# Kernel tuning notes

Measured on AMD Instinct MI355X. Metric: run time of the kernel, lower is better.

Reference implementation:

```python
import jax, jax.numpy as jnp
import numpy as np

B, P, S = 128, 10, 8
L, BF = 81, 75
OF, MF2 = 40, 20
C = 64
H = 3 * C  # hidden_size = 192
NCHAR = 8
EPS = 1e-5


def setup_inputs() -> dict:
    key = jax.random.key(0)
    ks = jax.random.split(key, 24)
    n = lambda i, shp: jax.random.normal(ks[i], shp, jnp.float32)
    w = lambda i, shp: jax.random.normal(ks[i], shp, jnp.float32) * 0.02
    return {
        "board": n(0, (B, P, S, L, BF)),
        "order": n(1, (B, P, S, OF)),
        "message": n(2, (B, P, S, MF2)),
        "other_ind": jax.random.uniform(ks[3], (B, P, 7), jnp.float32),
        "me_ind": jax.random.uniform(ks[4], (B, P, 7), jnp.float32),
        "h0": n(5, (P, B, H)),
        "c0": n(6, (P, B, H)),
        "Wb1": w(7, (1024, L * BF)), "bb1": jnp.zeros((1024,), jnp.float32),
        "Wb2": w(8, (256, 1024)), "bb2": jnp.zeros((256,), jnp.float32),
        "Wb3": w(9, (C, 256)), "bb3": jnp.zeros((C,), jnp.float32),
        "Wo1": w(10, (128, OF)), "bo1": jnp.zeros((128,), jnp.float32),
        "Wo2": w(11, (32, 128)), "bo2": jnp.zeros((32,), jnp.float32),
        "Wo3": w(12, (C, 32)), "bo3": jnp.zeros((C,), jnp.float32),
        "Wm1": w(13, (64, MF2)), "bm1": jnp.zeros((64,), jnp.float32),
        "Wm2": w(14, (32, 64)), "bm2": jnp.zeros((32,), jnp.float32),
        "Wm3": w(15, (C, 32)), "bm3": jnp.zeros((C,), jnp.float32),
        "g1": jnp.ones((C,), jnp.float32), "be1": jnp.zeros((C,), jnp.float32),
        "g2": jnp.ones((C,), jnp.float32), "be2": jnp.zeros((C,), jnp.float32),
        "g3": jnp.ones((C,), jnp.float32), "be3": jnp.zeros((C,), jnp.float32),
        "Wih": w(16, (4 * H, H)), "Whh": w(17, (4 * H, H)),
        "bih": jnp.zeros((4 * H,), jnp.float32), "bhh": jnp.zeros((4 * H,), jnp.float32),
        "Wf1": w(18, (256, S * H)), "bf1": jnp.zeros((256,), jnp.float32),
        "Wf2": w(19, (NCHAR, 256 + 14)), "bf2": jnp.zeros((NCHAR,), jnp.float32),
    }


def _mlp3(x, W1, b1, W2, b2, W3, b3):
    x = jax.nn.relu(x @ W1.T + b1)
    x = jax.nn.relu(x @ W2.T + b2)
    return x @ W3.T + b3


def _bn_relu(x, g, b):
    # x: [b, C, S]; BatchNorm1d in training mode -> biased batch stats over (N, L)
    m = x.mean(axis=(0, 2), keepdims=True)
    v = jnp.mean((x - m) ** 2, axis=(0, 2), keepdims=True)
    return jax.nn.relu(g[None, :, None] * (x - m) * jax.lax.rsqrt(v + EPS) + b[None, :, None])


def _forward(board, order, message, other_ind, me_ind, h0, c0,
             Wb1, bb1, Wb2, bb2, Wb3, bb3, Wo1, bo1, Wo2, bo2, Wo3, bo3,
             Wm1, bm1, Wm2, bm2, Wm3, bm3, g1, be1, g2, be2, g3, be3,
             Wih, Whh, bih, bhh, Wf1, bf1, Wf2, bf2):
    num_step = board.shape[2]

    def per_past(board_p, order_p, msg_p, oi_p, mi_p, h, c):
        bb = board_p.shape[0]
        bf = _mlp3(board_p.reshape(bb * num_step, -1), Wb1, bb1, Wb2, bb2, Wb3, bb3)
        bf = _bn_relu(jnp.swapaxes(bf.reshape(bb, num_step, -1), 1, 2), g1, be1)
        of = _mlp3(order_p.reshape(bb * num_step, -1), Wo1, bo1, Wo2, bo2, Wo3, bo3)
        of = _bn_relu(jnp.swapaxes(of.reshape(bb, num_step, -1), 1, 2), g2, be2)
        mf = _mlp3(msg_p.reshape(bb * num_step, -1), Wm1, bm1, Wm2, bm2, Wm3, bm3)
        mf = _bn_relu(jnp.swapaxes(mf.reshape(bb, num_step, -1), 1, 2), g3, be3)
        x_feat = jnp.concatenate([bf, of, mf], axis=-1)              # [b, C, 3S]
        x_feat = jnp.transpose(jnp.swapaxes(x_feat, 1, 2), (2, 0, 1))  # [C, b, 3S]
        x_feat = x_feat.reshape(num_step, bb, -1)                    # [S, b, H] (same C-order reindex as torch)

        def step(carry, xt):
            h_, c_ = carry
            gates = xt @ Wih.T + bih + h_ @ Whh.T + bhh
            i, f, g_, o = jnp.split(gates, 4, axis=-1)
            c_ = jax.nn.sigmoid(f) * c_ + jax.nn.sigmoid(i) * jnp.tanh(g_)
            h_ = jax.nn.sigmoid(o) * jnp.tanh(c_)
            return (h_, c_), h_

        _, outs = jax.lax.scan(step, (h, c), x_feat)  # [S, b, H]
        x = jnp.swapaxes(outs, 0, 1).reshape(bb, -1)  # [b, S*H]
        x = jax.nn.relu(x @ Wf1.T + bf1)
        x = jnp.concatenate([x, oi_p, mi_p], axis=-1)  # [b, 256+14]
        return x @ Wf2.T + bf2

    per = jax.vmap(per_past)(
        jnp.swapaxes(board, 0, 1), jnp.swapaxes(order, 0, 1), jnp.swapaxes(message, 0, 1),
        jnp.swapaxes(other_ind, 0, 1), jnp.swapaxes(me_ind, 0, 1), h0, c0)  # [P, b, NCHAR]
    return per.sum(axis=0)


def reference(board, order, message, other_ind, me_ind, h0, c0,
              Wb1, bb1, Wb2, bb2, Wb3, bb3, Wo1, bo1, Wo2, bo2, Wo3, bo3,
              Wm1, bm1, Wm2, bm2, Wm3, bm3, g1, be1, g2, be2, g3, be3,
              Wih, Whh, bih, bhh, Wf1, bf1, Wf2, bf2):
    return _forward(board, order, message, other_ind, me_ind, h0, c0,
                    Wb1, bb1, Wb2, bb2, Wb3, bb3, Wo1, bo1, Wo2, bo2, Wo3, bo3,
                    Wm1, bm1, Wm2, bm2, Wm3, bm3, g1, be1, g2, be2, g3, be3,
                    Wih, Whh, bih, bhh, Wf1, bf1, Wf2, bf2)
```

## Files before the change

kernel.cpp:

```cpp
#include <hip/hip_runtime.h>
#include <stdint.h>

typedef unsigned short u16;
typedef __bf16 v8bf __attribute__((ext_vector_type(8)));
typedef float  v4f  __attribute__((ext_vector_type(4)));

__device__ __forceinline__ u16 f2bf(float f) {
    union { float f; unsigned u; } x; x.f = f;
    unsigned r = (x.u + 0x7FFFu + ((x.u >> 16) & 1u)) >> 16;
    return (u16)r;
}
__device__ __forceinline__ float sigf(float x) { return 1.f / (1.f + __expf(-x)); }
__device__ __forceinline__ void gload(const u16* src, u16* ldst) {
    __builtin_amdgcn_global_load_lds((const __attribute__((address_space(1))) void*)src,
                                     (__attribute__((address_space(3))) void*)ldst, 16, 0, 0);
}

#define OFF_ABF    0UL
#define OFF_XINBF  0UL
#define OFF_XG     3932160UL
#define OFF_FC1    44728320UL
#define OFF_WB1    125829120UL
#define OFF_C1     138412032UL
#define OFF_WB2    159383552UL
#define OFF_WB3    165150720UL
#define OFF_BFE    165216256UL
#define OFF_OFE    167837696UL
#define OFF_MFE    170459136UL
#define OFF_WIH    173095936UL
#define OFF_WHH    173390848UL
#define OFF_WF1    173685760UL
#define OFF_BSUM   174472192UL

__global__ void __launch_bounds__(256) conv_board(const float* __restrict__ src, u16* __restrict__ dst)
{
    int bid = blockIdx.x;
    int row = bid / 6, chunk = bid - row * 6;
    int k0 = chunk * 1024 + threadIdx.x * 4;
    const float* s = src + (long)row * 6075 + k0;
    u16* d = dst + (long)row * 6144 + k0;
    if (k0 + 4 <= 6075) {
        float f0 = s[0], f1 = s[1], f2 = s[2], f3 = s[3];
        uint2 v;
        v.x = (unsigned)f2bf(f0) | ((unsigned)f2bf(f1) << 16);
        v.y = (unsigned)f2bf(f2) | ((unsigned)f2bf(f3) << 16);
        *(uint2*)d = v;
    } else {
#pragma unroll
        for (int z = 0; z < 4; ++z) {
            int k = k0 + z;
            d[z] = f2bf(k < 6075 ? s[z] : 0.f);
        }
    }
}

__global__ void __launch_bounds__(256) conv_weights(
    const float* __restrict__ Wb1, const float* __restrict__ Wb2, const float* __restrict__ Wb3,
    const float* __restrict__ Wih, const float* __restrict__ Whh, const float* __restrict__ Wf1,
    const float* __restrict__ bih, const float* __restrict__ bhh,
    u16* __restrict__ dWb1, u16* __restrict__ dWb2, u16* __restrict__ dWb3,
    u16* __restrict__ dWih, u16* __restrict__ dWhh, u16* __restrict__ dWf1,
    float* __restrict__ bsum)
{
    const long C0 = 6291456, C1 = 6553600, C2 = 6586368, C3 = 6733824,
               C4 = 6881280, C5 = 7274496, C6 = 7275264;
    for (long i = (long)blockIdx.x * 256 + threadIdx.x; i < C6; i += (long)gridDim.x * 256) {
        if (i < C0) {
            int r = (int)(i / 6144), k = (int)(i % 6144);
            dWb1[i] = f2bf(k < 6075 ? Wb1[(long)r * 6075 + k] : 0.f);
        } else if (i < C1) {
            long j = i - C0;
            dWb2[j] = f2bf(Wb2[j]);
        } else if (i < C2) {
            long j = i - C1;
            dWb3[j] = f2bf(j < 16384 ? Wb3[j] : 0.f);
        } else if (i < C3) {
            long j = i - C2;
            dWih[j] = f2bf(Wih[j]);
        } else if (i < C4) {
            long j = i - C3;
            dWhh[j] = f2bf(Whh[j]);
        } else if (i < C5) {
            long j = i - C4;
            dWf1[j] = f2bf(Wf1[j]);
        } else {
            long j = i - C5;
            bsum[j] = bih[j] + bhh[j];
        }
    }
}

#define G160_LDS 106496
__global__ void __launch_bounds__(512, 1)
gemm160(const u16* __restrict__ A, const u16* __restrict__ B,
        const float* __restrict__ bias, u16* __restrict__ C, int K)
{
    extern __shared__ __align__(16) u16 smem[];
    const int tid = threadIdx.x, wv = tid >> 6, lane = tid & 63;
    const int bid = blockIdx.x;
    const int col = bid >> 6, rowt = bid & 63;
    const long m0 = (long)rowt * 160;
    const long n0 = (long)col * 256;

    const int sr8 = lane >> 3;
    const int sslot = (lane & 7) ^ sr8;
    const u16* Ag = A + (m0 + wv * 8 + sr8) * (long)K + sslot * 8;
    const u16* Bg = B + (n0 + wv * 8 + sr8) * (long)K + sslot * 8;
    const int wr = wv >> 2, wc = wv & 3;
    const int wm = wr * 80, wn = wc * 64;
    const int fr = lane & 15, hi = lane >> 4, fx = fr & 7;

    const int nk = K >> 6;
    v4f acc[5][4] = {};

    auto STAGE = [&](int buf, int t) {
        const long k0 = (long)t * 64;
        const int ab = buf * 26624;
#pragma unroll
        for (int r = 0; r < 2; ++r)
            gload(Ag + (long)r * 64 * K + k0, smem + ab + r * 4096 + wv * 512);
        if (wv < 4)
            gload(Ag + (long)128 * K + k0, smem + ab + 8192 + wv * 512);
#pragma unroll
        for (int r = 0; r < 4; ++r)
            gload(Bg + (long)r * 64 * K + k0, smem + ab + 10240 + r * 4096 + wv * 512);
    };
    auto LDA_ = [&](int buf, int ks, int i) -> v8bf {
        return *(const v8bf*)(smem + buf * 26624 + (wm + i * 16 + fr) * 64 + ((ks * 4 + hi) ^ fx) * 8);
    };
    auto LDB_ = [&](int buf, int ks, int j) -> v8bf {
        return *(const v8bf*)(smem + buf * 26624 + 10240 + (wn + j * 16 + fr) * 64 + ((ks * 4 + hi) ^ fx) * 8);
    };

    STAGE(0, 0);
    STAGE(1, 1);
    for (int t = 0; t < nk; ++t) {
        const int buf = t & 1;
        if (t + 1 < nk) { asm volatile("s_waitcnt vmcnt(6)" ::: "memory"); }
        else            { asm volatile("s_waitcnt vmcnt(0)" ::: "memory"); }
        asm volatile("s_barrier" ::: "memory");
        __builtin_amdgcn_s_setprio(1);
        v8bf a0[5], a1[5], b0[4], b1[4];
#pragma unroll
        for (int j = 0; j < 4; ++j) b0[j] = LDB_(buf, 0, j);
#pragma unroll
        for (int i = 0; i < 5; ++i) a0[i] = LDA_(buf, 0, i);
        __builtin_amdgcn_sched_barrier(0);
#pragma unroll
        for (int j = 0; j < 4; ++j) b1[j] = LDB_(buf, 1, j);
#pragma unroll
        for (int i = 0; i < 5; ++i) a1[i] = LDA_(buf, 1, i);
#pragma unroll
        for (int i = 0; i < 5; ++i)
#pragma unroll
            for (int j = 0; j < 4; ++j)
                acc[i][j] = __builtin_amdgcn_mfma_f32_16x16x32_bf16(a0[i], b0[j], acc[i][j], 0, 0, 0);
        __builtin_amdgcn_sched_barrier(0);
        __builtin_amdgcn_s_setprio(0);
        asm volatile("s_waitcnt lgkmcnt(0)" ::: "memory");
        __builtin_amdgcn_sched_barrier(0);
        asm volatile("s_barrier" ::: "memory");
        if (t + 2 < nk) STAGE(buf, t + 2);
        __builtin_amdgcn_s_setprio(1);
#pragma unroll
        for (int i = 0; i < 5; ++i)
#pragma unroll
            for (int j = 0; j < 4; ++j)
                acc[i][j] = __builtin_amdgcn_mfma_f32_16x16x32_bf16(a1[i], b1[j], acc[i][j], 0, 0, 0);
        __builtin_amdgcn_s_setprio(0);
    }

#pragma unroll
    for (int i = 0; i < 5; ++i) {
        const long mr = m0 + wm + i * 16 + hi * 4;
#pragma unroll
        for (int j = 0; j < 4; ++j) {
            const long n = n0 + wn + j * 16 + fr;
            float bv = bias[n];
#pragma unroll
            for (int r = 0; r < 4; ++r) {
                float v = fmaxf(acc[i][j][r] + bv, 0.f);
                C[(mr + r) * 1024L + n] = f2bf(v);
            }
        }
    }
}

#define L23_LDS 98304
__global__ void __launch_bounds__(512, 1)
gemm_l23(const u16* __restrict__ A, const u16* __restrict__ B, const float* __restrict__ b2,
         const u16* __restrict__ W3, const float* __restrict__ b3, float* __restrict__ Out)
{
    extern __shared__ __align__(16) u16 smem[];
    const int tid = threadIdx.x, wv = tid >> 6, lane = tid & 63;
    const long m0 = (long)blockIdx.x * 128;
    const int sr8 = lane >> 3;
    const int sslot = (lane & 7) ^ sr8;
    const u16* Ag = A + (m0 + wv * 8 + sr8) * 1024L + sslot * 8;
    const u16* Bg = B + (wv * 8 + sr8) * 1024L + sslot * 8;
    const int wr = wv >> 2, wc = wv & 3;
    const int wm = wr * 64, wn = wc * 64;
    const int fr = lane & 15, hi = lane >> 4, fx = fr & 7;

    v4f acc[4][4] = {};

    auto STAGE = [&](int buf, int t) {
        const long k0 = (long)t * 64;
        const int ab = buf * 24576;
#pragma unroll
        for (int r = 0; r < 2; ++r)
            gload(Ag + (long)r * 64 * 1024 + k0, smem + ab + r * 4096 + wv * 512);
#pragma unroll
        for (int r = 0; r < 4; ++r)
            gload(Bg + (long)r * 64 * 1024 + k0, smem + ab + 8192 + r * 4096 + wv * 512);
    };
    auto COMPUTE = [&](int buf) {
#pragma unroll
        for (int ks = 0; ks < 2; ++ks) {
            const int sw = ((ks * 4 + hi) ^ fx) * 8;
            v8bf a[4], b[4];
#pragma unroll
            for (int i = 0; i < 4; ++i)
                a[i] = *(const v8bf*)(smem + buf * 24576 + (wm + i * 16 + fr) * 64 + sw);
#pragma unroll
            for (int j = 0; j < 4; ++j)
                b[j] = *(const v8bf*)(smem + buf * 24576 + 8192 + (wn + j * 16 + fr) * 64 + sw);
#pragma unroll
            for (int i = 0; i < 4; ++i)
#pragma unroll
                for (int j = 0; j < 4; ++j)
                    acc[i][j] = __builtin_amdgcn_mfma_f32_16x16x32_bf16(a[i], b[j], acc[i][j], 0, 0, 0);
        }
    };

    STAGE(0, 0);
    __syncthreads();
    int t = 1;
    while (true) {
        if (t < 16) STAGE(1, t);
        COMPUTE(0);
        if (t >= 16) break;
        __syncthreads();
        ++t;
        if (t < 16) STAGE(0, t);
        COMPUTE(1);
        if (t >= 16) break;
        __syncthreads();
        ++t;
    }
    __syncthreads();
    u16* C2s = smem;
#pragma unroll
    for (int i = 0; i < 4; ++i) {
        const int rrow = wm + i * 16 + hi * 4;
#pragma unroll
        for (int j = 0; j < 4; ++j) {
            const int ccol = wn + j * 16 + fr;
            float bv = b2[ccol];
#pragma unroll
            for (int r = 0; r < 4; ++r)
                C2s[(rrow + r) * 264 + ccol] = f2bf(fmaxf(acc[i][j][r] + bv, 0.f));
        }
    }
    __syncthreads();
    v4f a3[4] = {};
#pragma unroll
    for (int kk = 0; kk < 8; ++kk) {
        v8bf af = *(const v8bf*)(&C2s[(wv * 16 + fr) * 264 + kk * 32 + hi * 8]);
#pragma unroll
        for (int j = 0; j < 4; ++j) {
            v8bf bfr = *(const v8bf*)(W3 + (j * 16 + fr) * 256 + kk * 32 + hi * 8);
            a3[j] = __builtin_amdgcn_mfma_f32_16x16x32_bf16(af, bfr, a3[j], 0, 0, 0);
        }
    }
#pragma unroll
    for (int j = 0; j < 4; ++j) {
        int n = j * 16 + fr;
        float bv = b3[n];
#pragma unroll
        for (int q = 0; q < 4; ++q)
            Out[(m0 + wv * 16 + hi * 4 + q) * 64 + n] = a3[j][q] + bv;
    }
}

template<int OBF, int RELU, int BIAS>
__global__ void __launch_bounds__(256)
gemm_bt(const u16* __restrict__ A, const u16* __restrict__ B,
        const float* __restrict__ bias, void* __restrict__ Cv,
        int M, int N, int K, int ldc)
{
    __shared__ __align__(16) u16 As[2][128 * 64];
    __shared__ __align__(16) u16 Bs[2][128 * 64];
    const int tid = threadIdx.x;
    const int wv = tid >> 6, lane = tid & 63;
    const long m0 = (long)blockIdx.y * 128;
    const long n0 = (long)blockIdx.x * 128;
    const int srow  = wv * 8 + (lane >> 3);
    const int sslot = (lane & 7) ^ (lane >> 3);
    const u16* Ag = A + (m0 + srow) * (long)K + sslot * 8;
    const u16* Bg = B + (n0 + srow) * (long)K + sslot * 8;
    const int wm = (wv >> 1) * 64, wn = (wv & 1) * 64;
    const int fr = lane & 15, hi = lane >> 4;
    const int fx = fr & 7;

    v4f acc[4][4] = {};
    const int nk = K >> 6;

    auto STAGE = [&](int buf, int k0) {
#pragma unroll
        for (int r = 0; r < 4; ++r)
            gload(Ag + (long)r * 32 * K + k0, &As[buf][r * 2048 + wv * 512]);
#pragma unroll
        for (int r = 0; r < 4; ++r)
            gload(Bg + (long)r * 32 * K + k0, &Bs[buf][r * 2048 + wv * 512]);
    };
    auto COMPUTE = [&](int buf) {
#pragma unroll
        for (int ks = 0; ks < 2; ++ks) {
            v8bf a[4], b[4];
            const int sw = (((ks * 4 + hi) ^ fx)) * 8;
#pragma unroll
            for (int i = 0; i < 4; ++i)
                a[i] = *(const v8bf*)(&As[buf][(wm + i * 16 + fr) * 64 + sw]);
#pragma unroll
            for (int j = 0; j < 4; ++j)
                b[j] = *(const v8bf*)(&Bs[buf][(wn + j * 16 + fr) * 64 + sw]);
#pragma unroll
            for (int i = 0; i < 4; ++i)
#pragma unroll
                for (int j = 0; j < 4; ++j)
                    acc[i][j] = __builtin_amdgcn_mfma_f32_16x16x32_bf16(a[i], b[j], acc[i][j], 0, 0, 0);
        }
    };

    STAGE(0, 0);
    __syncthreads();
    int t = 1;
    while (true) {
        if (t < nk) STAGE(1, t * 64);
        COMPUTE(0);
        if (t >= nk) break;
        __syncthreads();
        ++t;
        if (t < nk) STAGE(0, t * 64);
        COMPUTE(1);
        if (t >= nk) break;
        __syncthreads();
        ++t;
    }

#pragma unroll
    for (int i = 0; i < 4; ++i) {
        const long mr = m0 + wm + i * 16 + hi * 4;
#pragma unroll
        for (int j = 0; j < 4; ++j) {
            const long n = n0 + wn + j * 16 + fr;
            if (n < N) {
                float bv = BIAS ? bias[n] : 0.f;
#pragma unroll
                for (int r = 0; r < 4; ++r) {
                    float v = acc[i][j][r] + bv;
                    if (RELU) v = fmaxf(v, 0.f);
                    if (OBF) ((u16*)Cv)[(mr + r) * (long)ldc + n] = f2bf(v);
                    else     ((float*)Cv)[(mr + r) * (long)ldc + n] = v;
                }
            }
        }
    }
}

template<int D0, int D1>
__global__ void __launch_bounds__(256)
mlp3_small(const float* __restrict__ X,
           const float* __restrict__ W1, const float* __restrict__ B1,
           const float* __restrict__ W2, const float* __restrict__ B2,
           const float* __restrict__ W3, const float* __restrict__ B3,
           float* __restrict__ Out)
{
    __shared__ float w1s[D0 * D1];
    __shared__ float w2s[D1 * 32];
    __shared__ float w3s[32 * 64];
    __shared__ float b1s[D1], b2s[32], b3s[64];
    __shared__ float xs[32 * D0];
    __shared__ float h1[32 * D1];
    __shared__ float h2[32 * 32];

    const int tid = threadIdx.x;
    const long row0 = (long)blockIdx.x * 32;

    for (int i = tid; i < D0 * D1; i += 256) { int k = i / D1, n = i % D1; w1s[i] = W1[n * D0 + k]; }
    for (int i = tid; i < D1 * 32; i += 256) { int k = i / 32,  n = i % 32; w2s[i] = W2[n * D1 + k]; }
    for (int i = tid; i < 32 * 64; i += 256) { int k = i / 64,  n = i % 64; w3s[i] = W3[n * 32 + k]; }
    if (tid < D1) b1s[tid] = B1[tid];
    if (tid < 32) b2s[tid] = B2[tid];
    if (tid < 64) b3s[tid] = B3[tid];
    for (int i = tid; i < 32 * D0; i += 256) xs[i] = X[(row0 + i / D0) * D0 + i % D0];
    __syncthreads();

    const int wv = tid >> 6, lane = tid & 63;
    const int r0 = wv * 8;
    {
        constexpr int NL = D1 / 64;
        float acc[NL][8];
#pragma unroll
        for (int a = 0; a < NL; ++a)
#pragma unroll
            for (int r = 0; r < 8; ++r) acc[a][r] = 0.f;
        for (int k = 0; k < D0; ++k) {
            float w[NL];
#pragma unroll
            for (int a = 0; a < NL; ++a) w[a] = w1s[k * D1 + lane + a * 64];
#pragma unroll
            for (int r = 0; r < 8; ++r) {
                float x = xs[(r0 + r) * D0 + k];
#pragma unroll
                for (int a = 0; a < NL; ++a) acc[a][r] += w[a] * x;
            }
        }
#pragma unroll
        for (int a = 0; a < NL; ++a)
#pragma unroll
            for (int r = 0; r < 8; ++r)
                h1[(r0 + r) * D1 + lane + a * 64] = fmaxf(acc[a][r] + b1s[lane + a * 64], 0.f);
    }
    __syncthreads();
    {
        int n = lane & 31;
        int rb = r0 + (lane >> 5) * 4;
        float acc[4] = {0, 0, 0, 0};
        for (int k = 0; k < D1; ++k) {
            float w = w2s[k * 32 + n];
#pragma unroll
            for (int r = 0; r < 4; ++r) acc[r] += w * h1[(rb + r) * D1 + k];
        }
#pragma unroll
        for (int r = 0; r < 4; ++r) h2[(rb + r) * 32 + n] = fmaxf(acc[r] + b2s[n], 0.f);
    }
    __syncthreads();
    {
        float acc[8] = {};
        for (int k = 0; k < 32; ++k) {
            float w = w3s[k * 64 + lane];
#pragma unroll
            for (int r = 0; r < 8; ++r) acc[r] += w * h2[(r0 + r) * 32 + k];
        }
#pragma unroll
        for (int r = 0; r < 8; ++r) Out[(row0 + r0 + r) * 64 + lane] = acc[r] + b3s[lane];
    }
}

#define BX_LDS 100032
__global__ void __launch_bounds__(256, 1)
build_xin2(const float* __restrict__ bfe, const float* __restrict__ ofe, const float* __restrict__ mfe,
           const float* __restrict__ g1, const float* __restrict__ be1,
           const float* __restrict__ g2, const float* __restrict__ be2,
           const float* __restrict__ g3, const float* __restrict__ be3,
           u16* __restrict__ xin)
{
    extern __shared__ __align__(16) float ls[];
    float* coefA = ls + 24576;
    float* coefB = coefA + 24;
    float* psum  = coefB + 24;
    float* psum2 = psum + 192;
    const int p = blockIdx.x >> 3, s = blockIdx.x & 7;
    const int tid = threadIdx.x;
    const float* Fs[3] = {bfe, ofe, mfe};
    for (int g = tid; g < 3072; g += 256) {
        int br = g >> 10, rr = g & 1023, bb = rr >> 3, tt = rr & 7;
        const float* srcp = Fs[br] + ((long)(bb * 80 + p * 8 + tt)) * 64 + s * 8;
        float4 v0 = *(const float4*)srcp;
        float4 v1 = *(const float4*)(srcp + 4);
        *(float4*)(ls + (long)g * 8) = v0;
        *(float4*)(ls + (long)g * 8 + 4) = v1;
    }
    __syncthreads();
    if (tid < 192) {
        int pair = tid >> 3, part = tid & 7;
        int br = pair >> 3, cl = pair & 7;
        float s1 = 0.f, s2 = 0.f;
        for (int b2 = 0; b2 < 16; ++b2) {
            int bb = part * 16 + b2;
            const float* base = ls + ((br * 128 + bb) * 8) * 8 + cl;
#pragma unroll
            for (int tt = 0; tt < 8; ++tt) { float v = base[tt * 8]; s1 += v; s2 += v * v; }
        }
        psum[tid] = s1; psum2[tid] = s2;
    }
    __syncthreads();
    if (tid < 24) {
        float s1 = 0.f, s2 = 0.f;
#pragma unroll
        for (int q = 0; q < 8; ++q) { s1 += psum[tid * 8 + q]; s2 += psum2[tid * 8 + q]; }
        int br = tid >> 3, cl = tid & 7, c = s * 8 + cl;
        const float* G  = br == 0 ? g1  : (br == 1 ? g2  : g3);
        const float* BE = br == 0 ? be1 : (br == 1 ? be2 : be3);
        float m  = s1 * (1.f / 1024.f);
        float var = s2 * (1.f / 1024.f) - m * m;
        float Aa = G[c] * rsqrtf(var + 1e-5f);
        coefA[tid] = Aa;
        coefB[tid] = BE[c] - Aa * m;
    }
    __syncthreads();
    const int u = tid >> 1, h0 = (tid & 1) * 96;
    const long obase = ((long)(p * 8 + s) * 128 + u) * 192 + h0;
    const int cl = u >> 4;
    const int ub = (u & 15) * 8;
    union { u16 u[8]; uint4 v; } pk;
    for (int hq = 0; hq < 12; ++hq) {
#pragma unroll
        for (int z = 0; z < 8; ++z) {
            int h = h0 + hq * 8 + z;
            int bb = ub + h / 24, t = h % 24, br = t >> 3, tt = t & 7;
            float v = ls[((br * 128 + bb) * 8 + tt) * 8 + cl];
            float r = fmaxf(v * coefA[br * 8 + cl] + coefB[br * 8 + cl], 0.f);
            pk.u[z] = f2bf(r);
        }
        *(uint4*)(xin + obase + hq * 8) = pk.v;
    }
}

#define LSTM_LDS (98304 + 6400 + 49152)
__global__ void __launch_bounds__(512, 1)
lstm_persist(const float* __restrict__ Xg, const u16* __restrict__ Whh,
             const float* __restrict__ h0, const float* __restrict__ c0,
             const u16* __restrict__ Wf1, const float* __restrict__ bf1,
             float* __restrict__ fc1o)
{
    extern __shared__ __align__(16) u16 smem[];
    u16*   WT    = smem;
    u16*   hS    = smem + 2 * 128 * 192;
    float* gates = (float*)(smem + 2 * 128 * 192 + 16 * 200);

    const int tid = threadIdx.x, wv = tid >> 6, lane = tid & 63;
    const int R0 = blockIdx.x * 16;
    const int fr = lane & 15, hi = lane >> 4;

    for (int i = tid; i < 16 * 200; i += 512) {
        int r = i / 200, cx = i % 200;
        hS[i] = (cx < 192) ? f2bf(h0[(R0 + r) * 192 + cx]) : (u16)0;
    }
    float creg[6];
#pragma unroll
    for (int j = 0; j < 6; ++j) {
        int e = j * 512 + tid;
        creg[j] = c0[(R0 + e / 192) * 192 + e % 192];
    }

    auto WSTAGE = [&](int buf, int it) {
#pragma unroll
        for (int q = 0; q < 6; ++q) {
            int g = q * 512 + tid;
            int row = g / 24, sl = g % 24;
            const u16* src = Whh + (long)(it * 128 + row) * 192 + (sl ^ (row & 7)) * 8;
            gload(src, WT + buf * 24576 + q * 4096 + wv * 512);
        }
    };
    auto NITER = [&](int buf, int nt, const v8bf* a) {
        int row = wv * 16 + fr;
        v4f acc = {};
#pragma unroll
        for (int ks = 0; ks < 6; ++ks) {
            v8bf b = *(const v8bf*)(&WT[buf * 24576 + row * 192 + ((ks * 4 + hi) ^ (fr & 7)) * 8]);
            acc = __builtin_amdgcn_mfma_f32_16x16x32_bf16(a[ks], b, acc, 0, 0, 0);
        }
        int n = nt * 128 + row;
#pragma unroll
        for (int q = 0; q < 4; ++q)
            gates[(hi * 4 + q) * 768 + n] = acc[q];
    };

    v4f f1acc[2] = {};
    const int nb0 = wv * 32;
    auto WF1ACC = [&](int ss, const v8bf* a) {
#pragma unroll
        for (int jf = 0; jf < 2; ++jf) {
            v4f tacc = f1acc[jf];
#pragma unroll
            for (int ks = 0; ks < 6; ++ks) {
                v8bf bfr = *(const v8bf*)(Wf1 + (long)(nb0 + jf * 16 + fr) * 1536 + ss * 192 + ks * 32 + hi * 8);
                tacc = __builtin_amdgcn_mfma_f32_16x16x32_bf16(a[ks], bfr, tacc, 0, 0, 0);
            }
            f1acc[jf] = tacc;
        }
    };

    WSTAGE(0, 0);
    for (int s = 0; s < 8; ++s) {
        __syncthreads();
        v8bf a[6];
#pragma unroll
        for (int ks = 0; ks < 6; ++ks)
            a[ks] = *(const v8bf*)(&hS[fr * 200 + ks * 32 + hi * 8]);
        if (s > 0) WF1ACC(s - 1, a);
        int it = 0;
#pragma unroll 1
        for (int pr = 0; pr < 3; ++pr) {
            WSTAGE(1, it + 1);
            NITER(0, it, a);
            __syncthreads();
            if (it + 2 < 6) WSTAGE(0, it + 2);
            else if (s < 7) WSTAGE(0, 0);
            NITER(1, it + 1, a);
            __syncthreads();
            it += 2;
        }
#pragma unroll
        for (int j = 0; j < 6; ++j) {
            int e = j * 512 + tid;
            int r = e / 192, hd = e % 192;
            int grow = R0 + r;
            int p = grow >> 7, u = grow & 127;
            long xrow = (long)((p * 8 + s) * 128 + u) * 768;
            float gi = Xg[xrow + hd]       + gates[r * 768 + hd];
            float gf = Xg[xrow + 192 + hd] + gates[r * 768 + 192 + hd];
            float gg = Xg[xrow + 384 + hd] + gates[r * 768 + 384 + hd];
            float go = Xg[xrow + 576 + hd] + gates[r * 768 + 576 + hd];
            float c = sigf(gf) * creg[j] + sigf(gi) * tanhf(gg);
            float h = sigf(go) * tanhf(c);
            creg[j] = c;
            hS[r * 200 + hd] = f2bf(h);
        }
    }
    __syncthreads();
    {
        v8bf a[6];
#pragma unroll
        for (int ks = 0; ks < 6; ++ks)
            a[ks] = *(const v8bf*)(&hS[fr * 200 + ks * 32 + hi * 8]);
        WF1ACC(7, a);
    }
#pragma unroll
    for (int jf = 0; jf < 2; ++jf)
#pragma unroll
        for (int q = 0; q < 4; ++q) {
            int row = hi * 4 + q;
            int n = nb0 + jf * 16 + fr;
            fc1o[(long)(R0 + row) * 256 + n] = fmaxf(f1acc[jf][q] + bf1[n], 0.f);
        }
}

__global__ void __launch_bounds__(256) final_fc2(
    const float* __restrict__ fc1, const float* __restrict__ oi, const float* __restrict__ mi,
    const float* __restrict__ Wf2, const float* __restrict__ bf2, float* __restrict__ out)
{
    const int wv = threadIdx.x >> 6, lane = threadIdx.x & 63;
    const int w = blockIdx.x * 4 + wv;
    const int u = w >> 3, n = w & 7;
    const float* wrow = Wf2 + n * 270;
    float wreg[4];
#pragma unroll
    for (int q = 0; q < 4; ++q) wreg[q] = wrow[lane + 64 * q];
    float wtail = (lane < 14) ? wrow[256 + lane] : 0.f;
    float acc = 0.f;
    for (int p = 0; p < 10; ++p) {
        const float* x = fc1 + (long)(p * 128 + u) * 256;
#pragma unroll
        for (int q = 0; q < 4; ++q) acc += x[lane + 64 * q] * wreg[q];
        float t = 0.f;
        if (lane < 7)       t = oi[(u * 10 + p) * 7 + lane];
        else if (lane < 14) t = mi[(u * 10 + p) * 7 + lane - 7];
        acc += t * wtail;
    }
#pragma unroll
    for (int off = 32; off; off >>= 1) acc += __shfl_xor(acc, off);
    if (lane == 0) out[u * 8 + n] = acc + bf2[n];
}

extern "C" void kernel_launch(void* const* d_in, const int* in_sizes, int n_in,
                              void* d_out, int out_size, void* d_ws, size_t ws_size,
                              hipStream_t stream)
{
    (void)in_sizes; (void)n_in; (void)out_size; (void)ws_size;
    const float* board = (const float*)d_in[0];
    const float* order = (const float*)d_in[1];
    const float* mess  = (const float*)d_in[2];
    const float* oi    = (const float*)d_in[3];
    const float* mi    = (const float*)d_in[4];
    const float* h0    = (const float*)d_in[5];
    const float* c0    = (const float*)d_in[6];
    const float* Wb1 = (const float*)d_in[7];  const float* bb1 = (const float*)d_in[8];
    const float* Wb2 = (const float*)d_in[9];  const float* bb2 = (const float*)d_in[10];
    const float* Wb3 = (const float*)d_in[11]; const float* bb3 = (const float*)d_in[12];
    const float* Wo1 = (const float*)d_in[13]; const float* bo1 = (const float*)d_in[14];
    const float* Wo2 = (const float*)d_in[15]; const float* bo2 = (const float*)d_in[16];
    const float* Wo3 = (const float*)d_in[17]; const float* bo3 = (const float*)d_in[18];
    const float* Wm1 = (const float*)d_in[19]; const float* bm1 = (const float*)d_in[20];
    const float* Wm2 = (const float*)d_in[21]; const float* bm2 = (const float*)d_in[22];
    const float* Wm3 = (const float*)d_in[23]; const float* bm3 = (const float*)d_in[24];
    const float* g1  = (const float*)d_in[25]; const float* be1 = (const float*)d_in[26];
    const float* g2  = (const float*)d_in[27]; const float* be2 = (const float*)d_in[28];
    const float* g3  = (const float*)d_in[29]; const float* be3 = (const float*)d_in[30];
    const float* Wih = (const float*)d_in[31]; const float* Whh = (const float*)d_in[32];
    const float* bih = (const float*)d_in[33]; const float* bhh = (const float*)d_in[34];
    const float* Wf1 = (const float*)d_in[35]; const float* bf1 = (const float*)d_in[36];
    const float* Wf2 = (const float*)d_in[37]; const float* bf2 = (const float*)d_in[38];

    uint8_t* ws = (uint8_t*)d_ws;
    u16*   A_bf    = (u16*)(ws + OFF_ABF);
    u16*   xin_bf  = (u16*)(ws + OFF_XINBF);
    float* Xg      = (float*)(ws + OFF_XG);
    float* fc1o    = (float*)(ws + OFF_FC1);
    u16*   Wb1_bf  = (u16*)(ws + OFF_WB1);
    u16*   C1_bf   = (u16*)(ws + OFF_C1);
    u16*   Wb2_bf  = (u16*)(ws + OFF_WB2);
    u16*   Wb3_bf  = (u16*)(ws + OFF_WB3);
    float* bfe     = (float*)(ws + OFF_BFE);
    float* ofe     = (float*)(ws + OFF_OFE);
    float* mfe     = (float*)(ws + OFF_MFE);
    u16*   Wih_bf  = (u16*)(ws + OFF_WIH);
    u16*   Whh_bf  = (u16*)(ws + OFF_WHH);
    u16*   Wf1_bf  = (u16*)(ws + OFF_WF1);
    float* bsum    = (float*)(ws + OFF_BSUM);

    conv_board<<<61440, 256, 0, stream>>>(board, A_bf);
    conv_weights<<<2048, 256, 0, stream>>>(Wb1, Wb2, Wb3, Wih, Whh, Wf1, bih, bhh,
                                           Wb1_bf, Wb2_bf, Wb3_bf, Wih_bf, Whh_bf, Wf1_bf, bsum);

    hipFuncSetAttribute(reinterpret_cast<const void*>(gemm160),
                        hipFuncAttributeMaxDynamicSharedMemorySize, G160_LDS);
    gemm160<<<256, 512, G160_LDS, stream>>>(A_bf, Wb1_bf, bb1, C1_bf, 6144);
    hipFuncSetAttribute(reinterpret_cast<const void*>(gemm_l23),
                        hipFuncAttributeMaxDynamicSharedMemorySize, L23_LDS);
    gemm_l23<<<80, 512, L23_LDS, stream>>>(C1_bf, Wb2_bf, bb2, Wb3_bf, bb3, bfe);

    mlp3_small<40, 128><<<320, 256, 0, stream>>>(order, Wo1, bo1, Wo2, bo2, Wo3, bo3, ofe);
    mlp3_small<20, 64><<<320, 256, 0, stream>>>(mess,  Wm1, bm1, Wm2, bm2, Wm3, bm3, mfe);

    hipFuncSetAttribute(reinterpret_cast<const void*>(build_xin2),
                        hipFuncAttributeMaxDynamicSharedMemorySize, BX_LDS);
    build_xin2<<<80, 256, BX_LDS, stream>>>(bfe, ofe, mfe, g1, be1, g2, be2, g3, be3, xin_bf);

    gemm_bt<0, 0, 1><<<dim3(6, 80), 256, 0, stream>>>(xin_bf, Wih_bf, bsum, Xg, 10240, 768, 192, 768);

    hipFuncSetAttribute(reinterpret_cast<const void*>(lstm_persist),
                        hipFuncAttributeMaxDynamicSharedMemorySize, LSTM_LDS);
    lstm_persist<<<80, 512, LSTM_LDS, stream>>>(Xg, Whh_bf, h0, c0, Wf1_bf, bf1, fc1o);

    final_fc2<<<256, 256, 0, stream>>>(fc1o, oi, mi, Wf2, bf2, (float*)d_out);
}
```

Before: 410.2 us.

## Keep LSTM recurrent weights in registers and retile board GEMM for two blocks per CU

The LSTM kernel now loads its per-wave slice of Whh into registers once (36 bf16 fragments per lane) and drops the per-timestep double-buffered LDS staging, along with most barriers inside the recurrence. The first board GEMM is retiled from 512-thread blocks with 160x256 tiles to 256-thread blocks with 160x128 tiles, using less LDS and launch bounds that allow two blocks per CU. Both changes aim to cut memory traffic and synchronisation stalls. The risks are register pressure and spilling in the LSTM kernel, and doubled B-matrix reloads or changed vmcnt accounting in the GEMM.

Measured after the change: 412.1 us. No clear change (+0.5%).

```diff
diff --git a/kernel.cpp b/kernel.cpp
--- a/kernel.cpp
+++ b/kernel.cpp
@@ -90,23 +90,23 @@
     }
 }
 
-#define G160_LDS 106496
-__global__ void __launch_bounds__(512, 1)
+#define G160_LDS 73728
+__global__ void __launch_bounds__(256, 2)
 gemm160(const u16* __restrict__ A, const u16* __restrict__ B,
         const float* __restrict__ bias, u16* __restrict__ C, int K)
 {
     extern __shared__ __align__(16) u16 smem[];
     const int tid = threadIdx.x, wv = tid >> 6, lane = tid & 63;
     const int bid = blockIdx.x;
-    const int col = bid >> 6, rowt = bid & 63;
+    const int col = bid & 7, rowt = bid >> 3;
     const long m0 = (long)rowt * 160;
-    const long n0 = (long)col * 256;
+    const long n0 = (long)col * 128;
 
     const int sr8 = lane >> 3;
     const int sslot = (lane & 7) ^ sr8;
     const u16* Ag = A + (m0 + wv * 8 + sr8) * (long)K + sslot * 8;
     const u16* Bg = B + (n0 + wv * 8 + sr8) * (long)K + sslot * 8;
-    const int wr = wv >> 2, wc = wv & 3;
+    const int wr = wv >> 1, wc = wv & 1;
     const int wm = wr * 80, wn = wc * 64;
     const int fr = lane & 15, hi = lane >> 4, fx = fr & 7;
 
@@ -115,28 +115,26 @@
 
     auto STAGE = [&](int buf, int t) {
         const long k0 = (long)t * 64;
-        const int ab = buf * 26624;
-#pragma unroll
-        for (int r = 0; r < 2; ++r)
-            gload(Ag + (long)r * 64 * K + k0, smem + ab + r * 4096 + wv * 512);
-        if (wv < 4)
-            gload(Ag + (long)128 * K + k0, smem + ab + 8192 + wv * 512);
+        const int ab = buf * 18432;
+#pragma unroll
+        for (int r = 0; r < 5; ++r)
+            gload(Ag + (long)r * 32 * K + k0, smem + ab + r * 2048 + wv * 512);
 #pragma unroll
         for (int r = 0; r < 4; ++r)
-            gload(Bg + (long)r * 64 * K + k0, smem + ab + 10240 + r * 4096 + wv * 512);
+            gload(Bg + (long)r * 32 * K + k0, smem + ab + 10240 + r * 2048 + wv * 512);
     };
     auto LDA_ = [&](int buf, int ks, int i) -> v8bf {
-        return *(const v8bf*)(smem + buf * 26624 + (wm + i * 16 + fr) * 64 + ((ks * 4 + hi) ^ fx) * 8);
+        return *(const v8bf*)(smem + buf * 18432 + (wm + i * 16 + fr) * 64 + ((ks * 4 + hi) ^ fx) * 8);
     };
     auto LDB_ = [&](int buf, int ks, int j) -> v8bf {
-        return *(const v8bf*)(smem + buf * 26624 + 10240 + (wn + j * 16 + fr) * 64 + ((ks * 4 + hi) ^ fx) * 8);
+        return *(const v8bf*)(smem + buf * 18432 + 10240 + (wn + j * 16 + fr) * 64 + ((ks * 4 + hi) ^ fx) * 8);
     };
 
     STAGE(0, 0);
     STAGE(1, 1);
     for (int t = 0; t < nk; ++t) {
         const int buf = t & 1;
-        if (t + 1 < nk) { asm volatile("s_waitcnt vmcnt(6)" ::: "memory"); }
+        if (t + 1 < nk) { asm volatile("s_waitcnt vmcnt(9)" ::: "memory"); }
         else            { asm volatile("s_waitcnt vmcnt(0)" ::: "memory"); }
         asm volatile("s_barrier" ::: "memory");
         __builtin_amdgcn_s_setprio(1);
@@ -519,7 +517,7 @@
     }
 }
 
-#define LSTM_LDS (98304 + 6400 + 49152)
+#define LSTM_LDS (6400 + 49152)
 __global__ void __launch_bounds__(512, 1)
 lstm_persist(const float* __restrict__ Xg, const u16* __restrict__ Whh,
              const float* __restrict__ h0, const float* __restrict__ c0,
@@ -527,14 +525,20 @@
              float* __restrict__ fc1o)
 {
     extern __shared__ __align__(16) u16 smem[];
-    u16*   WT    = smem;
-    u16*   hS    = smem + 2 * 128 * 192;
-    float* gates = (float*)(smem + 2 * 128 * 192 + 16 * 200);
+    u16*   hS    = smem;
+    float* gates = (float*)(smem + 16 * 200);
 
     const int tid = threadIdx.x, wv = tid >> 6, lane = tid & 63;
     const int R0 = blockIdx.x * 16;
     const int fr = lane & 15, hi = lane >> 4;
 
+    v8bf Wreg[6][6];
+#pragma unroll
+    for (int nt = 0; nt < 6; ++nt)
+#pragma unroll
+        for (int ks = 0; ks < 6; ++ks)
+            Wreg[nt][ks] = *(const v8bf*)(Whh + (long)(nt * 128 + wv * 16 + fr) * 192 + ks * 32 + hi * 8);
+
     for (int i = tid; i < 16 * 200; i += 512) {
         int r = i / 200, cx = i % 200;
         hS[i] = (cx < 192) ? f2bf(h0[(R0 + r) * 192 + cx]) : (u16)0;
@@ -545,29 +549,6 @@
         int e = j * 512 + tid;
         creg[j] = c0[(R0 + e / 192) * 192 + e % 192];
     }
-
-    auto WSTAGE = [&](int buf, int it) {
-#pragma unroll
-        for (int q = 0; q < 6; ++q) {
-            int g = q * 512 + tid;
-            int row = g / 24, sl = g % 24;
-            const u16* src = Whh + (long)(it * 128 + row) * 192 + (sl ^ (row & 7)) * 8;
-            gload(src, WT + buf * 24576 + q * 4096 + wv * 512);
-        }
-    };
-    auto NITER = [&](int buf, int nt, const v8bf* a) {
-        int row = wv * 16 + fr;
-        v4f acc = {};
-#pragma unroll
-        for (int ks = 0; ks < 6; ++ks) {
-            v8bf b = *(const v8bf*)(&WT[buf * 24576 + row * 192 + ((ks * 4 + hi) ^ (fr & 7)) * 8]);
-            acc = __builtin_amdgcn_mfma_f32_16x16x32_bf16(a[ks], b, acc, 0, 0, 0);
-        }
-        int n = nt * 128 + row;
-#pragma unroll
-        for (int q = 0; q < 4; ++q)
-            gates[(hi * 4 + q) * 768 + n] = acc[q];
-    };
 
     v4f f1acc[2] = {};
     const int nb0 = wv * 32;
@@ -584,7 +565,6 @@
         }
     };
 
-    WSTAGE(0, 0);
     for (int s = 0; s < 8; ++s) {
         __syncthreads();
         v8bf a[6];
@@ -592,18 +572,18 @@
         for (int ks = 0; ks < 6; ++ks)
             a[ks] = *(const v8bf*)(&hS[fr * 200 + ks * 32 + hi * 8]);
         if (s > 0) WF1ACC(s - 1, a);
-        int it = 0;
-#pragma unroll 1
-        for (int pr = 0; pr < 3; ++pr) {
-            WSTAGE(1, it + 1);
-            NITER(0, it, a);
-            __syncthreads();
-            if (it + 2 < 6) WSTAGE(0, it + 2);
-            else if (s < 7) WSTAGE(0, 0);
-            NITER(1, it + 1, a);
-            __syncthreads();
-            it += 2;
-        }
+#pragma unroll
+        for (int nt = 0; nt < 6; ++nt) {
+            v4f acc = {};
+#pragma unroll
+            for (int ks = 0; ks < 6; ++ks)
+                acc = __builtin_amdgcn_mfma_f32_16x16x32_bf16(a[ks], Wreg[nt][ks], acc, 0, 0, 0);
+            int n = nt * 128 + wv * 16 + fr;
+#pragma unroll
+            for (int q = 0; q < 4; ++q)
+                gates[(hi * 4 + q) * 768 + n] = acc[q];
+        }
+        __syncthreads();
 #pragma unroll
         for (int j = 0; j < 6; ++j) {
             int e = j * 512 + tid;
@@ -718,7 +698,7 @@
 
     hipFuncSetAttribute(reinterpret_cast<const void*>(gemm160),
                         hipFuncAttributeMaxDynamicSharedMemorySize, G160_LDS);
-    gemm160<<<256, 512, G160_LDS, stream>>>(A_bf, Wb1_bf, bb1, C1_bf, 6144);
+    gemm160<<<512, 256, G160_LDS, stream>>>(A_bf, Wb1_bf, bb1, C1_bf, 6144);
     hipFuncSetAttribute(reinterpret_cast<const void*>(gemm_l23),
                         hipFuncAttributeMaxDynamicSharedMemorySize, L23_LDS);
     gemm_l23<<<80, 512, L23_LDS, stream>>>(C1_bf, Wb2_bf, bb2, Wb3_bf, bb3, bfe);
```
